# Performance work log

Measured on AMD Instinct MI355X. Metric: run time of the kernel, lower is better.

## Reference

```python
import jax, jax.numpy as jnp
import numpy as np

B, S, D, H = 4, 2048, 256, 8  # batch, seq, d_hidden (= per-head dim), n_heads
ROPE_BASE = 10000.0


def _rope_tables(seq_len, dim, dtype=jnp.float32):
    # standard RoPE: inv_freq over half the dim, half-split rotate
    inv_freq = 1.0 / (ROPE_BASE ** (jnp.arange(0, dim, 2, dtype=jnp.float32) / dim))
    angles = jnp.arange(seq_len, dtype=jnp.float32)[:, None] * inv_freq[None, :]  # [S, D/2]
    return jnp.cos(angles).astype(dtype), jnp.sin(angles).astype(dtype)


def _apply_rope(x, cos, sin):
    # x: [..., S, D]; cos/sin: [S, D/2]
    d2 = x.shape[-1] // 2
    x1, x2 = x[..., :d2], x[..., d2:]
    return jnp.concatenate([x1 * cos - x2 * sin, x1 * sin + x2 * cos], axis=-1)


def setup_inputs() -> dict:
    key = jax.random.key(0)
    ks = jax.random.split(key, 5)
    scale_in = 1.0 / np.sqrt(D)
    scale_out = 1.0 / np.sqrt(H * D)
    return {
        "x": jax.random.normal(ks[0], (B, S, D), jnp.float32),
        "w_qkv": jax.random.normal(ks[1], (3 * H * D, D), jnp.float32) * scale_in,
        "b_qkv": jax.random.normal(ks[2], (3 * H * D,), jnp.float32) * 0.02,
        "w_out": jax.random.normal(ks[3], (D, H * D), jnp.float32) * scale_out,
        "b_out": jax.random.normal(ks[4], (D,), jnp.float32) * 0.02,
    }


def reference(x, w_qkv, b_qkv, w_out, b_out):
    b, s, d = x.shape
    # QKV projection: [b, s, 3*H*D]
    qkv = x @ w_qkv.T + b_qkv
    # einops '(qkv heads hidden)': qkv axis outermost -> [b, s, 3, H, D]
    qkv = qkv.reshape(b, s, 3, H, D)
    qkv = jnp.transpose(qkv, (2, 0, 3, 1, 4))  # [3, b, H, s, D]
    q, k, v = qkv[0], qkv[1], qkv[2]
    cos, sin = _rope_tables(s, D, x.dtype)
    q = _apply_rope(q, cos, sin)
    k = _apply_rope(k, cos, sin)
    # non-causal SDPA, scale = 1/sqrt(D)
    scores = jnp.einsum('bhqd,bhkd->bhqk', q, k) / jnp.sqrt(jnp.asarray(D, x.dtype))
    probs = jax.nn.softmax(scores, axis=-1)
    attn = jnp.einsum('bhqk,bhkd->bhqd', probs, v)  # [b, H, s, D]
    # '... heads seq hidden -> ... seq (heads hidden)'
    attn_concat = jnp.transpose(attn, (0, 2, 1, 3)).reshape(b, s, H * D)
    out = attn_concat @ w_out.T + b_out
    return x + out
```

## Files before the change

### kernel.cpp

```cpp
#include <hip/hip_runtime.h>
#include <hip/hip_bf16.h>
#include <stdint.h>

#define Sq   2048
#define Dq   256
#define Hq   8
#define NQKV 6144
#define HD   2048
#define MTOK 8192

typedef __attribute__((ext_vector_type(8))) short short8;
typedef __attribute__((ext_vector_type(4))) float f32x4;
typedef __attribute__((ext_vector_type(16))) float f32x16;
typedef __attribute__((ext_vector_type(4))) int i32x4;

__device__ __forceinline__ float bf2f(short v) {
  union { float f; unsigned u; } x; x.u = ((unsigned)(unsigned short)v) << 16; return x.f;
}
__device__ __forceinline__ short f2bf(float f) {
  union { float f; unsigned u; } x; x.f = f;
  unsigned r = x.u + 0x7fffu + ((x.u >> 16) & 1u);
  return (short)(r >> 16);
}
__device__ __forceinline__ void gload16(const void* g, void* lds) {
  auto g1 = (const __attribute__((address_space(1))) int*)(uintptr_t)g;
  auto l3 = (__attribute__((address_space(3))) int*)(uintptr_t)lds;
  __builtin_amdgcn_global_load_lds(g1, l3, 16, 0, 0);
}
__device__ __forceinline__ float exp2a(float x) {
  float r; asm("v_exp_f32 %0, %1" : "=v"(r) : "v"(x)); return r;
}
__device__ __forceinline__ unsigned cvtpk(float lo, float hi) {
  unsigned r; asm("v_cvt_pk_bf16_f32 %0, %1, %2" : "=v"(r) : "v"(lo), "v"(hi)); return r;
}
__device__ __forceinline__ void plswap(unsigned &a, unsigned &b) {
  asm volatile("v_permlane32_swap_b32 %0, %1" : "+v"(a), "+v"(b));
}
__device__ __forceinline__ f32x16 fz16() {
  f32x16 z;
#pragma unroll
  for (int e = 0; e < 16; e++) z[e] = 0.f;
  return z;
}

__global__ __launch_bounds__(256) void k_prep(
    const float* __restrict__ x, const float* __restrict__ wqkv,
    const float* __restrict__ wout,
    short* __restrict__ xb, short* __restrict__ wqb, short* __restrict__ wob,
    float* __restrict__ cost, float* __restrict__ sint)
{
  long i = (long)blockIdx.x * 256 + threadIdx.x;
  const long n_x  = (long)MTOK * Dq;
  const long n_wq = (long)NQKV * Dq;
  const long n_wo = (long)Dq * HD;
  const long n_tab = (long)Sq * 128;
  if (i < n_x) { xb[i] = f2bf(x[i]); return; }
  i -= n_x;
  if (i < n_wq) { wqb[i] = f2bf(wqkv[i]); return; }
  i -= n_wq;
  if (i < n_wo) { wob[i] = f2bf(wout[i]); return; }
  i -= n_wo;
  if (i < n_tab) {
    int s = (int)(i >> 7), j = (int)(i & 127);
    float inv = __expf(-(float)j * (9.2103403720f / 128.0f));
    float a = (float)s * inv;
    cost[i] = cosf(a);
    sint[i] = sinf(a);
  }
}

template<int EPI, int BN>
__global__ __launch_bounds__(256, 2) void k_gemm(
    const short* __restrict__ A, const short* __restrict__ Bt,
    const float* __restrict__ bias, const float* __restrict__ resid,
    void* __restrict__ Cp, int M, int N, int K)
{
  constexpr int MI = (BN == 128) ? 4 : 2;
  constexpr int WRS = MI * 16;
  constexpr int BROUNDS = BN / 32;
  __shared__ short As[128 * 64];
  __shared__ short Bs[BN * 64];
  const int tid = threadIdx.x;
  const int w = tid >> 6, lane = tid & 63;
  const int grp = lane >> 4, l15 = lane & 15;
  const int wr = (BN == 128) ? (w >> 1) : w;
  const int wc = (BN == 128) ? (w & 1) : 0;
  const int m0 = blockIdx.y * 128, n0 = blockIdx.x * BN;

  f32x4 acc[MI][4];
#pragma unroll
  for (int i = 0; i < MI; i++)
#pragma unroll
    for (int j = 0; j < 4; j++) acc[i][j] = f32x4{0.f, 0.f, 0.f, 0.f};

  for (int kt = 0; kt < K; kt += 64) {
#pragma unroll
    for (int r = 0; r < 4; r++) {
      int G = r * 256 + tid;
      int row = G >> 3, gc = G & 7;
      gload16(A + (size_t)(m0 + row) * K + kt + gc * 8,
              (char*)As + (r * 256 + w * 64) * 16);
    }
#pragma unroll
    for (int r = 0; r < BROUNDS; r++) {
      int G = r * 256 + tid;
      int row = G >> 3, gc = G & 7;
      gload16(Bt + (size_t)(n0 + row) * K + kt + gc * 8,
              (char*)Bs + (r * 256 + w * 64) * 16);
    }
    __syncthreads();
#pragma unroll
    for (int kk = 0; kk < 2; kk++) {
      short8 af[MI], bf[4];
#pragma unroll
      for (int mi = 0; mi < MI; mi++) {
        int row = wr * WRS + mi * 16 + l15;
        af[mi] = *(const short8*)&As[row * 64 + kk * 32 + grp * 8];
      }
#pragma unroll
      for (int ni = 0; ni < 4; ni++) {
        int row = wc * 64 + ni * 16 + l15;
        bf[ni] = *(const short8*)&Bs[row * 64 + kk * 32 + grp * 8];
      }
#pragma unroll
      for (int mi = 0; mi < MI; mi++)
#pragma unroll
        for (int ni = 0; ni < 4; ni++)
          acc[mi][ni] = __builtin_amdgcn_mfma_f32_16x16x32_bf16(
              af[mi], bf[ni], acc[mi][ni], 0, 0, 0);
    }
    __syncthreads();
  }
#pragma unroll
  for (int mi = 0; mi < MI; mi++) {
#pragma unroll
    for (int ni = 0; ni < 4; ni++) {
      int colb = n0 + wc * 64 + ni * 16 + l15;
      float bv = bias[colb];
#pragma unroll
      for (int j = 0; j < 4; j++) {
        int row = m0 + wr * WRS + mi * 16 + grp * 4 + j;
        float v = acc[mi][ni][j] + bv;
        if (EPI == 0) {
          ((short*)Cp)[(size_t)row * N + colb] = f2bf(v);
        } else {
          size_t o = (size_t)row * N + colb;
          ((float*)Cp)[o] = v + resid[o];
        }
      }
    }
  }
}

__global__ __launch_bounds__(256) void k_rope(
    short* __restrict__ qkv, const float* __restrict__ cost,
    const float* __restrict__ sint)
{
  int id = blockIdx.x * 256 + threadIdx.x;
  int jv = id & 15;
  int h = (id >> 4) & 7;
  int t = id >> 7;
  int s = t & (Sq - 1);
  const float QS = 0.090168441f;
  size_t base = (size_t)t * NQKV + h * 256 + jv * 8;
  short8 q1 = *(const short8*)&qkv[base];
  short8 q2 = *(const short8*)&qkv[base + 128];
  short8 k1 = *(const short8*)&qkv[base + 2048];
  short8 k2 = *(const short8*)&qkv[base + 2048 + 128];
  const float* cp = &cost[(size_t)s * 128 + jv * 8];
  const float* sp = &sint[(size_t)s * 128 + jv * 8];
  short8 oq1, oq2, ok1, ok2;
#pragma unroll
  for (int e = 0; e < 8; e++) {
    float c = cp[e], sn = sp[e];
    float a = bf2f(q1[e]), b2 = bf2f(q2[e]);
    oq1[e] = f2bf((a * c - b2 * sn) * QS);
    oq2[e] = f2bf((a * sn + b2 * c) * QS);
    float ka = bf2f(k1[e]), kb = bf2f(k2[e]);
    ok1[e] = f2bf(ka * c - kb * sn);
    ok2[e] = f2bf(ka * sn + kb * c);
  }
  *(short8*)&qkv[base] = oq1;
  *(short8*)&qkv[base + 128] = oq2;
  *(short8*)&qkv[base + 2048] = ok1;
  *(short8*)&qkv[base + 2048 + 128] = ok2;
}

__global__ __launch_bounds__(256) void k_vt(
    const short* __restrict__ qkv, short* __restrict__ vT)
{
  __shared__ short t[64][72];
  int kt = blockIdx.x, dt = blockIdx.y, bh = blockIdx.z;
  int b = bh >> 3, h = bh & 7;
  int tid = threadIdx.x;
  int r = tid >> 2, c0 = (tid & 3) * 16;
  const short* src = &qkv[(size_t)(b * Sq + kt * 64 + r) * NQKV + 4096 + h * 256 + dt * 64 + c0];
  short8 v0 = *(const short8*)src;
  short8 v1 = *(const short8*)(src + 8);
#pragma unroll
  for (int e = 0; e < 8; e++) { t[r][c0 + e] = v0[e]; t[r][c0 + 8 + e] = v1[e]; }
  __syncthreads();
  short8 o0, o1;
#pragma unroll
  for (int e = 0; e < 8; e++) { o0[e] = t[c0 + e][r]; o1[e] = t[c0 + 8 + e][r]; }
  short* dst = &vT[(size_t)(bh * 256 + dt * 64 + r) * Sq + kt * 64 + c0];
  *(short8*)dst = o0;
  *(short8*)(dst + 8) = o1;
}

__global__ __launch_bounds__(256, 2) void k_attn(
    const short* __restrict__ qkv, const short* __restrict__ vT,
    short* __restrict__ attn)
{
  __shared__ short Ks[2][8192];
  __shared__ short Vs[2][8192];
  const int tid = threadIdx.x;
  const int w = tid >> 6, lane = tid & 63;
  const int l31 = lane & 31, hi = lane >> 5;
  const int id = blockIdx.x;
  const int bh = (id & 7) * 4 + ((id >> 3) & 3);
  const int qb0 = (id >> 5) * 128;
  const int b = bh >> 3, h = bh & 7;

  short8 qf[16];
  {
    const short* qbase = &qkv[(size_t)(b * Sq + qb0 + w * 32 + l31) * NQKV + h * 256 + hi * 8];
#pragma unroll
    for (int kc = 0; kc < 16; kc++) qf[kc] = *(const short8*)&qbase[kc * 16];
  }
  f32x16 o[8];
#pragma unroll
  for (int dt = 0; dt < 8; dt++) o[dt] = fz16();
  float m = -3e38f, l = 0.f;

  const size_t krow0 = (size_t)(b * Sq) * NQKV + 2048 + h * 256;
  const short* vbase = &vT[(size_t)bh * 256 * Sq];

#pragma unroll
  for (int r = 0; r < 4; r++) {
    int G = r * 256 + tid;
    gload16(&qkv[krow0 + (size_t)(G & 31) * NQKV + (G >> 5) * 8],
            (char*)&Ks[0][0] + (r * 256 + w * 64) * 16);
  }
  {
    short8 v0[4];
#pragma unroll
    for (int r = 0; r < 4; r++) {
      int G = r * 256 + tid;
      v0[r] = *(const short8*)&vbase[(size_t)(G >> 2) * Sq + (G & 3) * 8];
    }
#pragma unroll
    for (int r = 0; r < 4; r++) {
      int G = r * 256 + tid;
      int s = ((G & 3) << 8) | (G >> 2);
      *(short8*)&Vs[0][s * 8] = v0[r];
    }
  }
  __syncthreads();

  int cur = 0;
  for (int kt = 0; kt < Sq / 32; kt++) {
    short8 vnext[4];
    if (kt + 1 < Sq / 32) {
#pragma unroll
      for (int r = 0; r < 4; r++) {
        int G = r * 256 + tid;
        gload16(&qkv[krow0 + (size_t)((kt + 1) * 32 + (G & 31)) * NQKV + (G >> 5) * 8],
                (char*)&Ks[cur ^ 1][0] + (r * 256 + w * 64) * 16);
      }
#pragma unroll
      for (int r = 0; r < 4; r++) {
        int G = r * 256 + tid;
        vnext[r] = *(const short8*)&vbase[(size_t)(G >> 2) * Sq + (kt + 1) * 32 + (G & 3) * 8];
      }
    }

    f32x16 sc = fz16();
    __builtin_amdgcn_s_setprio(1);
#pragma unroll
    for (int kc = 0; kc < 16; kc++) {
      short8 ka = *(const short8*)&Ks[cur][((kc * 2 + hi) * 32 + l31) * 8];
      sc = __builtin_amdgcn_mfma_f32_32x32x16_bf16(ka, qf[kc], sc, 0, 0, 0);
    }
    __builtin_amdgcn_s_setprio(0);

    float t8[8];
#pragma unroll
    for (int e = 0; e < 8; e++) t8[e] = fmaxf(sc[e], sc[e + 8]);
#pragma unroll
    for (int e = 0; e < 4; e++) t8[e] = fmaxf(t8[e], t8[e + 4]);
    t8[0] = fmaxf(t8[0], t8[2]); t8[1] = fmaxf(t8[1], t8[3]);
    float pmax = fmaxf(t8[0], t8[1]);
    pmax = fmaxf(pmax, __shfl_xor(pmax, 32, 64));
    if (!__all(pmax <= m + 8.0f)) {
      float nm = fmaxf(m, pmax);
      float f = exp2a(m - nm);
      l *= f;
#pragma unroll
      for (int dt = 0; dt < 8; dt++)
#pragma unroll
        for (int e = 0; e < 16; e++) o[dt][e] *= f;
      m = nm;
    }
#pragma unroll
    for (int e = 0; e < 16; e++) sc[e] = exp2a(sc[e] - m);
    float r8[8];
#pragma unroll
    for (int e = 0; e < 8; e++) r8[e] = sc[e] + sc[e + 8];
#pragma unroll
    for (int e = 0; e < 4; e++) r8[e] = r8[e] + r8[e + 4];
    r8[0] += r8[2]; r8[1] += r8[3];
    float rs = r8[0] + r8[1];
    rs += __shfl_xor(rs, 32, 64);
    l += rs;

    short8 pa[2];
    {
      unsigned x0 = cvtpk(sc[0], sc[1]);
      unsigned y0 = cvtpk(sc[4], sc[5]);
      unsigned x1 = cvtpk(sc[2], sc[3]);
      unsigned y1 = cvtpk(sc[6], sc[7]);
      plswap(x0, y0);
      plswap(x1, y1);
      i32x4 w0; w0[0] = x0; w0[1] = x1; w0[2] = y0; w0[3] = y1;
      pa[0] = __builtin_bit_cast(short8, w0);
      unsigned x2 = cvtpk(sc[8],  sc[9]);
      unsigned y2 = cvtpk(sc[12], sc[13]);
      unsigned x3 = cvtpk(sc[10], sc[11]);
      unsigned y3 = cvtpk(sc[14], sc[15]);
      plswap(x2, y2);
      plswap(x3, y3);
      i32x4 w1; w1[0] = x2; w1[1] = x3; w1[2] = y2; w1[3] = y3;
      pa[1] = __builtin_bit_cast(short8, w1);
    }

    __builtin_amdgcn_s_setprio(1);
#pragma unroll
    for (int dt = 0; dt < 8; dt++) {
#pragma unroll
      for (int ks = 0; ks < 2; ks++) {
        short8 vb = *(const short8*)&Vs[cur][(((ks * 2 + hi) << 8) | (dt * 32 + l31)) * 8];
        o[dt] = __builtin_amdgcn_mfma_f32_32x32x16_bf16(pa[ks], vb, o[dt], 0, 0, 0);
      }
    }
    __builtin_amdgcn_s_setprio(0);

    if (kt + 1 < Sq / 32) {
#pragma unroll
      for (int r = 0; r < 4; r++) {
        int G = r * 256 + tid;
        int s = ((G & 3) << 8) | (G >> 2);
        *(short8*)&Vs[cur ^ 1][s * 8] = vnext[r];
      }
    }
    __syncthreads();
    cur ^= 1;
  }

  float linv = 1.0f / l;
  float li[16];
#pragma unroll
  for (int e = 0; e < 16; e++)
    li[e] = __shfl(linv, (e & 3) + 8 * (e >> 2) + 4 * hi, 64);
  short* orow = &attn[(size_t)(b * Sq + qb0 + w * 32) * HD + h * 256 + l31];
#pragma unroll
  for (int dt = 0; dt < 8; dt++)
#pragma unroll
    for (int e = 0; e < 16; e++)
      orow[(size_t)((e & 3) + 8 * (e >> 2) + 4 * hi) * HD + dt * 32] = f2bf(o[dt][e] * li[e]);
}

extern "C" void kernel_launch(void* const* d_in, const int* in_sizes, int n_in,
                              void* d_out, int out_size, void* d_ws, size_t ws_size,
                              hipStream_t stream) {
  const float* x     = (const float*)d_in[0];
  const float* w_qkv = (const float*)d_in[1];
  const float* b_qkv = (const float*)d_in[2];
  const float* w_out = (const float*)d_in[3];
  const float* b_out = (const float*)d_in[4];
  float* out = (float*)d_out;

  char* ws = (char*)d_ws;
  short* qkv  = (short*)ws;
  short* vT   = (short*)(ws + 100663296);
  short* attn = (short*)(ws + 134217728);
  short* xb   = (short*)(ws + 167772160);
  short* wqb  = (short*)(ws + 171966464);
  short* wob  = (short*)(ws + 175112192);
  float* cost = (float*)(ws + 176160768);
  float* sint = (float*)(ws + 177209344);

  k_prep<<<dim3(17408), 256, 0, stream>>>(x, w_qkv, w_out, xb, wqb, wob, cost, sint);
  k_gemm<0, 128><<<dim3(NQKV / 128, MTOK / 128), 256, 0, stream>>>(
      xb, wqb, b_qkv, nullptr, qkv, MTOK, NQKV, Dq);
  k_rope<<<dim3(4096), 256, 0, stream>>>(qkv, cost, sint);
  k_vt<<<dim3(32, 4, 32), 256, 0, stream>>>(qkv, vT);
  k_attn<<<dim3(512), 256, 0, stream>>>(qkv, vT, attn);
  k_gemm<1, 64><<<dim3(Dq / 64, MTOK / 128), 256, 0, stream>>>(
      attn, wob, b_out, x, out, MTOK, Dq, HD);
}
```

Before: 340.5 us.

## Quantize RoPE'd Q/K to FP8 e4m3 and use FP8 MFMA for attention scores

The RoPE kernel now converts rotated Q and K to FP8 e4m3 with a software routine and packs them in place into the QKV buffer. The attention kernel loads these FP8 tiles and computes QK^T with the 32x32x16 fp8 MFMA, applying the softmax scale in the exp step instead of pre-scaling Q. This halves K bandwidth and LDS footprint and raises score-MFMA throughput. Separately, V tiles are now streamed straight into LDS with global_load_lds instead of staging through registers. The cost is reduced score precision from e4m3 quantization and a more expensive per-element conversion in the RoPE kernel.

After: 339.0 us. Within noise of the previous version (-0.4%).

```diff
diff --git a/kernel.cpp b/kernel.cpp
--- a/kernel.cpp
+++ b/kernel.cpp
@@ -21,6 +21,27 @@
   union { float f; unsigned u; } x; x.f = f;
   unsigned r = x.u + 0x7fffu + ((x.u >> 16) & 1u);
   return (short)(r >> 16);
+}
+__device__ __forceinline__ unsigned f2e4m3(float f) {
+  union { float f; unsigned u; } x; x.f = f;
+  unsigned sign = (x.u >> 24) & 0x80u;
+  float af = fabsf(f);
+  if (af >= 448.f) return sign | 0x7Eu;
+  if (af < 0.0009765625f) return sign;
+  int e = (int)((x.u >> 23) & 0xff) - 127;
+  int L = (e < -6) ? -9 : e - 3;
+  union { float f; unsigned u; } s1, s2;
+  s1.u = (unsigned)(127 - L) << 23;
+  s2.u = (unsigned)(127 + L) << 23;
+  float t = rintf(af * s1.f);
+  float val = t * s2.f;
+  if (val == 0.f) return sign;
+  union { float f; unsigned u; } y; y.f = val;
+  int e2 = (int)((y.u >> 23) & 0xff) - 127;
+  unsigned byte;
+  if (e2 < -6) byte = (unsigned)(val * 512.f);
+  else byte = ((unsigned)(e2 + 7) << 3) | ((y.u >> 20) & 7u);
+  return sign | byte;
 }
 __device__ __forceinline__ void gload16(const void* g, void* lds) {
   auto g1 = (const __attribute__((address_space(1))) int*)(uintptr_t)g;
@@ -152,38 +173,38 @@
   }
 }
 
-__global__ __launch_bounds__(256) void k_rope(
+__global__ __launch_bounds__(256) void k_ropef8(
     short* __restrict__ qkv, const float* __restrict__ cost,
     const float* __restrict__ sint)
 {
-  int id = blockIdx.x * 256 + threadIdx.x;
-  int jv = id & 15;
-  int h = (id >> 4) & 7;
-  int t = id >> 7;
-  int s = t & (Sq - 1);
-  const float QS = 0.090168441f;
-  size_t base = (size_t)t * NQKV + h * 256 + jv * 8;
-  short8 q1 = *(const short8*)&qkv[base];
-  short8 q2 = *(const short8*)&qkv[base + 128];
-  short8 k1 = *(const short8*)&qkv[base + 2048];
-  short8 k2 = *(const short8*)&qkv[base + 2048 + 128];
+  int tt = blockIdx.x * 2 + (threadIdx.x >> 7);
+  int i = threadIdx.x & 127;
+  int h = i >> 4, jv = i & 15;
+  int s = tt & (Sq - 1);
+  const short* qrow = qkv + (size_t)tt * NQKV + h * 256 + jv * 8;
+  short8 q1 = *(const short8*)qrow;
+  short8 q2 = *(const short8*)(qrow + 128);
+  short8 k1 = *(const short8*)(qrow + 2048);
+  short8 k2 = *(const short8*)(qrow + 2048 + 128);
   const float* cp = &cost[(size_t)s * 128 + jv * 8];
   const float* sp = &sint[(size_t)s * 128 + jv * 8];
-  short8 oq1, oq2, ok1, ok2;
+  unsigned long oq1 = 0, oq2 = 0, ok1 = 0, ok2 = 0;
 #pragma unroll
   for (int e = 0; e < 8; e++) {
     float c = cp[e], sn = sp[e];
     float a = bf2f(q1[e]), b2 = bf2f(q2[e]);
-    oq1[e] = f2bf((a * c - b2 * sn) * QS);
-    oq2[e] = f2bf((a * sn + b2 * c) * QS);
+    oq1 |= (unsigned long)f2e4m3(a * c - b2 * sn) << (8 * e);
+    oq2 |= (unsigned long)f2e4m3(a * sn + b2 * c) << (8 * e);
     float ka = bf2f(k1[e]), kb = bf2f(k2[e]);
-    ok1[e] = f2bf(ka * c - kb * sn);
-    ok2[e] = f2bf(ka * sn + kb * c);
-  }
-  *(short8*)&qkv[base] = oq1;
-  *(short8*)&qkv[base + 128] = oq2;
-  *(short8*)&qkv[base + 2048] = ok1;
-  *(short8*)&qkv[base + 2048 + 128] = ok2;
+    ok1 |= (unsigned long)f2e4m3(ka * c - kb * sn) << (8 * e);
+    ok2 |= (unsigned long)f2e4m3(ka * sn + kb * c) << (8 * e);
+  }
+  __syncthreads();
+  char* dst = (char*)qkv + (size_t)tt * 12288 + h * 256 + jv * 8;
+  *(unsigned long*)(dst)              = oq1;
+  *(unsigned long*)(dst + 128)        = oq2;
+  *(unsigned long*)(dst + 2048)       = ok1;
+  *(unsigned long*)(dst + 2048 + 128) = ok2;
 }
 
 __global__ __launch_bounds__(256) void k_vt(
@@ -209,10 +230,10 @@
 }
 
 __global__ __launch_bounds__(256, 2) void k_attn(
-    const short* __restrict__ qkv, const short* __restrict__ vT,
+    const char* __restrict__ qkvb, const short* __restrict__ vT,
     short* __restrict__ attn)
 {
-  __shared__ short Ks[2][8192];
+  __shared__ char  Ks[2][8192];
   __shared__ short Vs[2][8192];
   const int tid = threadIdx.x;
   const int w = tid >> 6, lane = tid & 63;
@@ -221,57 +242,50 @@
   const int bh = (id & 7) * 4 + ((id >> 3) & 3);
   const int qb0 = (id >> 5) * 128;
   const int b = bh >> 3, h = bh & 7;
-
-  short8 qf[16];
+  const float QS = 0.090168441f;
+
+  long qf[16];
   {
-    const short* qbase = &qkv[(size_t)(b * Sq + qb0 + w * 32 + l31) * NQKV + h * 256 + hi * 8];
-#pragma unroll
-    for (int kc = 0; kc < 16; kc++) qf[kc] = *(const short8*)&qbase[kc * 16];
+    const char* qbase = qkvb + (size_t)(b * Sq + qb0 + w * 32 + l31) * 12288 + h * 256 + hi * 8;
+#pragma unroll
+    for (int kc = 0; kc < 16; kc++) qf[kc] = *(const long*)(qbase + kc * 16);
   }
   f32x16 o[8];
 #pragma unroll
   for (int dt = 0; dt < 8; dt++) o[dt] = fz16();
   float m = -3e38f, l = 0.f;
 
-  const size_t krow0 = (size_t)(b * Sq) * NQKV + 2048 + h * 256;
+  const char* kbase = qkvb + (size_t)(b * Sq) * 12288 + 2048 + h * 256;
   const short* vbase = &vT[(size_t)bh * 256 * Sq];
 
+#pragma unroll
+  for (int r = 0; r < 2; r++) {
+    int G = r * 256 + tid;
+    gload16(kbase + (size_t)(G & 31) * 12288 + (G >> 5) * 16,
+            (char*)&Ks[0][0] + (r * 256 + w * 64) * 16);
+  }
 #pragma unroll
   for (int r = 0; r < 4; r++) {
     int G = r * 256 + tid;
-    gload16(&qkv[krow0 + (size_t)(G & 31) * NQKV + (G >> 5) * 8],
-            (char*)&Ks[0][0] + (r * 256 + w * 64) * 16);
-  }
-  {
-    short8 v0[4];
-#pragma unroll
-    for (int r = 0; r < 4; r++) {
-      int G = r * 256 + tid;
-      v0[r] = *(const short8*)&vbase[(size_t)(G >> 2) * Sq + (G & 3) * 8];
-    }
-#pragma unroll
-    for (int r = 0; r < 4; r++) {
-      int G = r * 256 + tid;
-      int s = ((G & 3) << 8) | (G >> 2);
-      *(short8*)&Vs[0][s * 8] = v0[r];
-    }
+    gload16(vbase + (size_t)(G & 255) * Sq + (G >> 8) * 8,
+            (char*)&Vs[0][0] + (r * 256 + w * 64) * 16);
   }
   __syncthreads();
 
   int cur = 0;
   for (int kt = 0; kt < Sq / 32; kt++) {
-    short8 vnext[4];
     if (kt + 1 < Sq / 32) {
+#pragma unroll
+      for (int r = 0; r < 2; r++) {
+        int G = r * 256 + tid;
+        gload16(kbase + (size_t)((kt + 1) * 32 + (G & 31)) * 12288 + (G >> 5) * 16,
+                (char*)&Ks[cur ^ 1][0] + (r * 256 + w * 64) * 16);
+      }
 #pragma unroll
       for (int r = 0; r < 4; r++) {
         int G = r * 256 + tid;
-        gload16(&qkv[krow0 + (size_t)((kt + 1) * 32 + (G & 31)) * NQKV + (G >> 5) * 8],
-                (char*)&Ks[cur ^ 1][0] + (r * 256 + w * 64) * 16);
-      }
-#pragma unroll
-      for (int r = 0; r < 4; r++) {
-        int G = r * 256 + tid;
-        vnext[r] = *(const short8*)&vbase[(size_t)(G >> 2) * Sq + (kt + 1) * 32 + (G & 3) * 8];
+        gload16(vbase + (size_t)(G & 255) * Sq + (kt + 1) * 32 + (G >> 8) * 8,
+                (char*)&Vs[cur ^ 1][0] + (r * 256 + w * 64) * 16);
       }
     }
 
@@ -279,8 +293,8 @@
     __builtin_amdgcn_s_setprio(1);
 #pragma unroll
     for (int kc = 0; kc < 16; kc++) {
-      short8 ka = *(const short8*)&Ks[cur][((kc * 2 + hi) * 32 + l31) * 8];
-      sc = __builtin_amdgcn_mfma_f32_32x32x16_bf16(ka, qf[kc], sc, 0, 0, 0);
+      long ka = *(const long*)&Ks[cur][(kc * 32 + l31) * 16 + hi * 8];
+      sc = __builtin_amdgcn_mfma_f32_32x32x16_fp8_fp8(ka, qf[kc], sc, 0, 0, 0);
     }
     __builtin_amdgcn_s_setprio(0);
 
@@ -292,8 +306,9 @@
     t8[0] = fmaxf(t8[0], t8[2]); t8[1] = fmaxf(t8[1], t8[3]);
     float pmax = fmaxf(t8[0], t8[1]);
     pmax = fmaxf(pmax, __shfl_xor(pmax, 32, 64));
-    if (!__all(pmax <= m + 8.0f)) {
-      float nm = fmaxf(m, pmax);
+    float pms = pmax * QS;
+    if (!__all(pms <= m + 8.0f)) {
+      float nm = fmaxf(m, pms);
       float f = exp2a(m - nm);
       l *= f;
 #pragma unroll
@@ -303,7 +318,7 @@
       m = nm;
     }
 #pragma unroll
-    for (int e = 0; e < 16; e++) sc[e] = exp2a(sc[e] - m);
+    for (int e = 0; e < 16; e++) sc[e] = exp2a(fmaf(sc[e], QS, -m));
     float r8[8];
 #pragma unroll
     for (int e = 0; e < 8; e++) r8[e] = sc[e] + sc[e + 8];
@@ -345,14 +360,6 @@
     }
     __builtin_amdgcn_s_setprio(0);
 
-    if (kt + 1 < Sq / 32) {
-#pragma unroll
-      for (int r = 0; r < 4; r++) {
-        int G = r * 256 + tid;
-        int s = ((G & 3) << 8) | (G >> 2);
-        *(short8*)&Vs[cur ^ 1][s * 8] = vnext[r];
-      }
-    }
     __syncthreads();
     cur ^= 1;
   }
@@ -393,9 +400,9 @@
   k_prep<<<dim3(17408), 256, 0, stream>>>(x, w_qkv, w_out, xb, wqb, wob, cost, sint);
   k_gemm<0, 128><<<dim3(NQKV / 128, MTOK / 128), 256, 0, stream>>>(
       xb, wqb, b_qkv, nullptr, qkv, MTOK, NQKV, Dq);
-  k_rope<<<dim3(4096), 256, 0, stream>>>(qkv, cost, sint);
+  k_ropef8<<<dim3(MTOK / 2), 256, 0, stream>>>(qkv, cost, sint);
   k_vt<<<dim3(32, 4, 32), 256, 0, stream>>>(qkv, vT);
-  k_attn<<<dim3(512), 256, 0, stream>>>(qkv, vT, attn);
+  k_attn<<<dim3(512), 256, 0, stream>>>((const char*)qkv, vT, attn);
   k_gemm<1, 64><<<dim3(Dq / 64, MTOK / 128), 256, 0, stream>>>(
       attn, wob, b_out, x, out, MTOK, Dq, HD);
 }
```
